# Performance work log

Hardware: AMD Instinct MI355X
Metric: run time of the kernel (lower is better)

The kernel has to match this reference:

```python
import jax, jax.numpy as jnp
import numpy as np

N = 100_000   # nodes
E = 1_600_000 # edges (avg degree 16)
IN_DIM = 128
OUT_DIM = 64
NEG_SLOPE = 0.2  # PyG GATConv default


def setup_inputs() -> dict:
    key = jax.random.key(0)
    k_x, k_ei, k_w, k_as, k_ad = jax.random.split(key, 5)
    x = jax.random.normal(k_x, (N, IN_DIM), dtype=jnp.float32)
    edge_index = jax.random.randint(k_ei, (2, E), 0, N, dtype=jnp.int32)
    # GATConv params (heads=1): linear weight, attention vectors, output bias
    W = jax.random.normal(k_w, (IN_DIM, OUT_DIM), dtype=jnp.float32) / np.sqrt(IN_DIM)
    a_src = jax.random.normal(k_as, (OUT_DIM,), dtype=jnp.float32) * 0.1
    a_dst = jax.random.normal(k_ad, (OUT_DIM,), dtype=jnp.float32) * 0.1
    bias = jnp.zeros((OUT_DIM,), dtype=jnp.float32)
    return {"x": x, "edge_index": edge_index, "W": W, "a_src": a_src, "a_dst": a_dst, "bias": bias}


def reference(x, edge_index, W, a_src, a_dst, bias):
    # PyG GATConv, heads=1, add_self_loops=True
    h = x @ W                                   # [N, OUT]
    loop = jnp.arange(N, dtype=edge_index.dtype)
    ei = jnp.concatenate([edge_index, jnp.stack([loop, loop])], axis=1)  # [2, E+N]
    src, dst = ei[0], ei[1]
    # per-node attention logits, gathered per edge
    alpha_s = h @ a_src                         # [N]
    alpha_d = h @ a_dst                         # [N]
    e = alpha_s[src] + alpha_d[dst]             # [E+N]
    e = jnp.where(e > 0, e, NEG_SLOPE * e)      # leaky_relu
    # segment softmax over edges sharing the same destination node
    m = jax.ops.segment_max(e, dst, num_segments=N)   # every node has a self loop
    ex = jnp.exp(e - m[dst])
    s = jax.ops.segment_sum(ex, dst, num_segments=N)
    alpha = ex / s[dst]                         # [E+N]
    # weighted scatter-add of source messages
    out = jax.ops.segment_sum(alpha[:, None] * h[src], dst, num_segments=N)  # [N, OUT]
    return out + bias
```

## Files before the change

### kernel.cpp

```cpp
#include <hip/hip_runtime.h>
#include <hip/hip_bf16.h>

#ifndef NEG_SLOPE
#define NEG_SLOPE 0.2f
#endif

#define GRP_SHIFT 9
#define GRP_SIZE 512
#define NGMAX 256
#define MS_CHUNK 4096
#define BKT_CAP 10240

typedef short bf16x8 __attribute__((ext_vector_type(8)));
typedef float f32x4 __attribute__((ext_vector_type(4)));

__device__ __forceinline__ unsigned short f2bf(float f) {
    union { float f; unsigned int u; } c; c.f = f;
    unsigned int r = (c.u + 0x7FFFu + ((c.u >> 16) & 1u)) >> 16;
    return (unsigned short)r;
}
__device__ __forceinline__ float bf2f(unsigned short u) {
    union { unsigned int u; float f; } c; c.u = ((unsigned int)u) << 16;
    return c.f;
}
__device__ __forceinline__ float bflo(unsigned int u) {
    union { unsigned int u; float f; } c; c.u = u << 16;
    return c.f;
}
__device__ __forceinline__ float bfhi(unsigned int u) {
    union { unsigned int u; float f; } c; c.u = u & 0xffff0000u;
    return c.f;
}

struct MsSmem {
    unsigned int pack[MS_CHUNK];
    unsigned char gtag[MS_CHUNK];
    int hist[NGMAX];
    int gb[NGMAX];
    int wsum[4];
};

__global__ __launch_bounds__(256) void ms_kernel(
    const int* __restrict__ ei, const float* __restrict__ W,
    unsigned short* __restrict__ wb, int* __restrict__ cursor,
    unsigned int* __restrict__ pairs, int E, int NG, int nchunk)
{
    __shared__ MsSmem sm;
    const int tid = threadIdx.x;

    if ((int)blockIdx.x == nchunk) {
        for (int idx = tid; idx < 8192; idx += 256) {
            const int n = idx >> 7;
            const int k = idx & 127;
            wb[idx] = f2bf(W[k * 64 + n]);
        }
        return;
    }

    unsigned int* ls_pack = sm.pack;
    unsigned char* ls_g = sm.gtag;
    int* ls_hist = sm.hist;
    int* ls_gb = sm.gb;
    int* ls_wsum = sm.wsum;

    const int cs = (int)blockIdx.x * MS_CHUNK;
    const int n = min(MS_CHUNK, E - cs);
    const int* srcp = ei + cs;
    const int* dstp = ei + E + cs;

    ls_hist[tid] = 0;
    __syncthreads();
    for (int i = tid; i < n; i += 256)
        atomicAdd(&ls_hist[dstp[i] >> GRP_SHIFT], 1);
    __syncthreads();

    const int h = ls_hist[tid];
    const int lane = tid & 63;
    int incl = h;
#pragma unroll
    for (int off = 1; off < 64; off <<= 1) {
        const int t = __shfl_up(incl, off);
        if (lane >= off) incl += t;
    }
    const int wv = tid >> 6;
    if (lane == 63) ls_wsum[wv] = incl;
    __syncthreads();
    int wpre = 0;
    for (int w = 0; w < wv; ++w) wpre += ls_wsum[w];
    const int excl = wpre + incl - h;
    if (tid < NG && h > 0) {
        const int old = atomicAdd(&cursor[tid], h);
        ls_gb[tid] = tid * BKT_CAP + old - excl;
    }
    __syncthreads();
    ls_hist[tid] = excl;
    __syncthreads();

    for (int i = tid; i < n; i += 256) {
        const int src = srcp[i];
        const int dst = dstp[i];
        const int g = dst >> GRP_SHIFT;
        const int idx = atomicAdd(&ls_hist[g], 1);
        ls_pack[idx] = ((unsigned int)src << GRP_SHIFT) | (unsigned int)(dst & (GRP_SIZE - 1));
        ls_g[idx] = (unsigned char)g;
    }
    __syncthreads();

    for (int i = tid; i < n; i += 256) {
        const int g = ls_g[i];
        const int pos = ls_gb[g] + i;
        if (pos < (g + 1) * BKT_CAP)
            pairs[pos] = ls_pack[i];
    }
}

__global__ __launch_bounds__(1024) void group_sort_kernel(
    const unsigned int* __restrict__ pairs, const int* __restrict__ cursor,
    unsigned int* __restrict__ meta, int* __restrict__ csr, int N)
{
    __shared__ int sdeg[GRP_SIZE];
    __shared__ int scur[GRP_SIZE];
    __shared__ int swsum[8];
    __shared__ int ssrc[BKT_CAP];
    const int g = blockIdx.x;
    const int tid = threadIdx.x;
    const int eb0 = g * BKT_CAP;
    const int cnt = min(cursor[g], BKT_CAP);

    if (tid < GRP_SIZE) sdeg[tid] = 0;
    __syncthreads();
    for (int i = tid; i < cnt; i += 1024)
        atomicAdd(&sdeg[pairs[eb0 + i] & (GRP_SIZE - 1)], 1);
    __syncthreads();

    int s = 0, incl = 0;
    if (tid < GRP_SIZE) {
        s = sdeg[tid];
        const int lane = tid & 63;
        incl = s;
#pragma unroll
        for (int off = 1; off < 64; off <<= 1) {
            const int t = __shfl_up(incl, off);
            if (lane >= off) incl += t;
        }
        if (lane == 63) swsum[tid >> 6] = incl;
    }
    __syncthreads();
    if (tid < GRP_SIZE) {
        int wpre = 0;
        const int wv = tid >> 6;
        for (int w = 0; w < wv; ++w) wpre += swsum[w];
        const int excl = wpre + incl - s;
        scur[tid] = excl;
        const int node = (g << GRP_SHIFT) + tid;
        if (node < N)
            meta[node] = ((unsigned int)(eb0 + excl) << 10) | (unsigned int)min(s, 1023);
    }
    __syncthreads();

    for (int i = tid; i < cnt; i += 1024) {
        const unsigned int p = pairs[eb0 + i];
        const int idx = atomicAdd(&scur[p & (GRP_SIZE - 1)], 1);
        ssrc[idx] = (int)(p >> GRP_SHIFT);
    }
    __syncthreads();
    for (int i = tid; i < cnt; i += 1024)
        csr[eb0 + i] = ssrc[i];
}

__global__ __launch_bounds__(256) void gemm_kernel(
    const float* __restrict__ x, const unsigned short* __restrict__ wb,
    const float* __restrict__ a_src, const float* __restrict__ a_dst,
    unsigned short* __restrict__ hb, float* __restrict__ as_,
    float* __restrict__ ad_, int N)
{
    __shared__ unsigned short xb[64 * 136];
    const int tid = threadIdx.x;
    const int r0 = (int)blockIdx.x * 64;

    for (int idx = tid; idx < 2048; idx += 256) {
        const int r = idx >> 5;
        const int c4 = idx & 31;
        const int row = r0 + r;
        float4 v = make_float4(0.f, 0.f, 0.f, 0.f);
        if (row < N) v = ((const float4*)(x + (size_t)row * 128))[c4];
        ushort4 o;
        o.x = f2bf(v.x); o.y = f2bf(v.y); o.z = f2bf(v.z); o.w = f2bf(v.w);
        *(ushort4*)(xb + r * 136 + c4 * 4) = o;
    }
    __syncthreads();

    const int wv = tid >> 6;
    const int lane = tid & 63;
    const int m16 = lane & 15;
    const int quad = lane >> 4;

    f32x4 acc[4];
#pragma unroll
    for (int ct = 0; ct < 4; ++ct) acc[ct] = (f32x4){0.f, 0.f, 0.f, 0.f};

    const unsigned short* xrow = xb + (wv * 16 + m16) * 136;
#pragma unroll
    for (int kq = 0; kq < 4; ++kq) {
        const int k0 = kq * 32;
        const bf16x8 a = *(const bf16x8*)(xrow + k0 + quad * 8);
#pragma unroll
        for (int ct = 0; ct < 4; ++ct) {
            const bf16x8 b = *(const bf16x8*)(wb + (ct * 16 + m16) * 128 + k0 + quad * 8);
            acc[ct] = __builtin_amdgcn_mfma_f32_16x16x32_bf16(a, b, acc[ct], 0, 0, 0);
        }
    }

#pragma unroll
    for (int ct = 0; ct < 4; ++ct) {
#pragma unroll
        for (int rg = 0; rg < 4; ++rg) {
            const int row = r0 + wv * 16 + quad * 4 + rg;
            if (row < N) hb[(size_t)row * 64 + ct * 16 + m16] = f2bf(acc[ct][rg]);
        }
    }

    float asv[4], adv[4];
#pragma unroll
    for (int ct = 0; ct < 4; ++ct) {
        asv[ct] = a_src[ct * 16 + m16];
        adv[ct] = a_dst[ct * 16 + m16];
    }
#pragma unroll
    for (int rg = 0; rg < 4; ++rg) {
        float ps = acc[0][rg] * asv[0] + acc[1][rg] * asv[1] +
                   acc[2][rg] * asv[2] + acc[3][rg] * asv[3];
        float pd = acc[0][rg] * adv[0] + acc[1][rg] * adv[1] +
                   acc[2][rg] * adv[2] + acc[3][rg] * adv[3];
#pragma unroll
        for (int off = 1; off < 16; off <<= 1) {
            ps += __shfl_xor(ps, off);
            pd += __shfl_xor(pd, off);
        }
        const int row = r0 + wv * 16 + quad * 4 + rg;
        if (m16 == 0 && row < N) { as_[row] = ps; ad_[row] = pd; }
    }
}

__device__ void aggregate_slow(
    const unsigned short* __restrict__ h, const float* __restrict__ as_,
    const float* __restrict__ ad_, const int* __restrict__ csr,
    const float* __restrict__ bias, float* __restrict__ out,
    int wid, int p0, int deg, int lane)
{
    const float adi = ad_[wid];
    float e0 = as_[wid] + adi;
    e0 = e0 > 0.f ? e0 : NEG_SLOPE * e0;
    float m = e0, ll = 1.f;
    float acc = bf2f(h[(size_t)wid * 64 + lane]);
    const int p1 = p0 + deg;
    for (int p = p0; p < p1; ++p) {
        const int sj = csr[p];
        float ee = as_[sj] + adi;
        ee = ee > 0.f ? ee : NEG_SLOPE * ee;
        const float nm = fmaxf(m, ee);
        const float sc = __expf(m - nm);
        const float pp = __expf(ee - nm);
        ll = ll * sc + pp;
        acc = acc * sc + pp * bf2f(h[(size_t)sj * 64 + lane]);
        m = nm;
    }
    out[(size_t)wid * 64 + lane] = acc / ll + bias[lane];
}

__global__ __launch_bounds__(256) void aggregate_kernel(
    const unsigned short* __restrict__ h, const float* __restrict__ as_,
    const float* __restrict__ ad_, const unsigned int* __restrict__ meta,
    const int* __restrict__ csr, const float* __restrict__ bias,
    float* __restrict__ out, int N)
{
    const int wbase = (blockIdx.x * 256 + threadIdx.x) >> 6;
    const int lane = threadIdx.x & 63;
    const int widA = wbase * 2;
    if (widA >= N) return;
    const int widB = widA + 1;
    const bool hasB = (widB < N);

    const unsigned int mtA = meta[widA];
    const unsigned int mtB = hasB ? meta[widB] : 0u;
    const int p0A = (int)(mtA >> 10), degA = (int)(mtA & 1023u);
    const int p0B = (int)(mtB >> 10), degB = (int)(mtB & 1023u);

    if (degA <= 63 && degB <= 63) {
        const float adiA = ad_[widA];
        const float adiB = hasB ? ad_[widB] : 0.f;
        float e0A = as_[widA] + adiA;
        e0A = e0A > 0.f ? e0A : NEG_SLOPE * e0A;
        float e0B = hasB ? as_[widB] + adiB : 0.f;
        e0B = e0B > 0.f ? e0B : NEG_SLOPE * e0B;

        int sA = widA, sB = hasB ? widB : widA;
        float eA = -1e30f, eB = -1e30f;
        if (lane < degA) {
            sA = csr[p0A + lane];
            const float t = as_[sA] + adiA;
            eA = t > 0.f ? t : NEG_SLOPE * t;
        } else if (lane == degA) {
            eA = e0A;
        }
        if (hasB) {
            if (lane < degB) {
                sB = csr[p0B + lane];
                const float t = as_[sB] + adiB;
                eB = t > 0.f ? t : NEG_SLOPE * t;
            } else if (lane == degB) {
                eB = e0B;
            }
        }

        float mA = eA, mB = eB;
#pragma unroll
        for (int off = 1; off < 64; off <<= 1) {
            mA = fmaxf(mA, __shfl_xor(mA, off));
            mB = fmaxf(mB, __shfl_xor(mB, off));
        }
        const float peA = __expf(eA - mA);
        const float peB = hasB ? __expf(eB - mB) : 0.f;
        float lA = peA, lB = peB;
#pragma unroll
        for (int off = 1; off < 64; off <<= 1) {
            lA += __shfl_xor(lA, off);
            lB += __shfl_xor(lB, off);
        }

        const int half = lane >> 5;
        const int l5 = lane & 31;
        const unsigned int* hb32 = (const unsigned int*)h;
        float a0 = 0.f, a1 = 0.f, b0 = 0.f, b1 = 0.f;
        const int npA = (degA + 2) >> 1;
        const int npB = hasB ? (degB + 2) >> 1 : 0;
        const int npMax = max(npA, npB);

        for (int jp = 0; jp < npMax; jp += 4) {
            const int sl0 = (jp    ) * 2 + half;
            const int sl1 = (jp + 1) * 2 + half;
            const int sl2 = (jp + 2) * 2 + half;
            const int sl3 = (jp + 3) * 2 + half;
            const int sa0 = __shfl(sA, sl0), sa1 = __shfl(sA, sl1);
            const int sa2 = __shfl(sA, sl2), sa3 = __shfl(sA, sl3);
            const int sb0 = __shfl(sB, sl0), sb1 = __shfl(sB, sl1);
            const int sb2 = __shfl(sB, sl2), sb3 = __shfl(sB, sl3);
            const float wa0 = __shfl(peA, sl0), wa1 = __shfl(peA, sl1);
            const float wa2 = __shfl(peA, sl2), wa3 = __shfl(peA, sl3);
            const float wb0 = __shfl(peB, sl0), wb1 = __shfl(peB, sl1);
            const float wb2 = __shfl(peB, sl2), wb3 = __shfl(peB, sl3);
            const unsigned int ua0 = hb32[sa0 * 32 + l5];
            const unsigned int ua1 = hb32[sa1 * 32 + l5];
            const unsigned int ua2 = hb32[sa2 * 32 + l5];
            const unsigned int ua3 = hb32[sa3 * 32 + l5];
            const unsigned int ub0 = hb32[sb0 * 32 + l5];
            const unsigned int ub1 = hb32[sb1 * 32 + l5];
            const unsigned int ub2 = hb32[sb2 * 32 + l5];
            const unsigned int ub3 = hb32[sb3 * 32 + l5];
            a0 += wa0 * bflo(ua0); a1 += wa0 * bfhi(ua0);
            a0 += wa1 * bflo(ua1); a1 += wa1 * bfhi(ua1);
            a0 += wa2 * bflo(ua2); a1 += wa2 * bfhi(ua2);
            a0 += wa3 * bflo(ua3); a1 += wa3 * bfhi(ua3);
            b0 += wb0 * bflo(ub0); b1 += wb0 * bfhi(ub0);
            b0 += wb1 * bflo(ub1); b1 += wb1 * bfhi(ub1);
            b0 += wb2 * bflo(ub2); b1 += wb2 * bfhi(ub2);
            b0 += wb3 * bflo(ub3); b1 += wb3 * bfhi(ub3);
        }
        a0 += __shfl_xor(a0, 32);
        a1 += __shfl_xor(a1, 32);
        b0 += __shfl_xor(b0, 32);
        b1 += __shfl_xor(b1, 32);
        if (half == 0) {
            const float2 bv = ((const float2*)bias)[l5];
            float2 oA;
            oA.x = a0 / lA + bv.x;
            oA.y = a1 / lA + bv.y;
            ((float2*)(out + (size_t)widA * 64))[l5] = oA;
            if (hasB) {
                float2 oB;
                oB.x = b0 / lB + bv.x;
                oB.y = b1 / lB + bv.y;
                ((float2*)(out + (size_t)widB * 64))[l5] = oB;
            }
        }
    } else {
        aggregate_slow(h, as_, ad_, csr, bias, out, widA, p0A, degA, lane);
        if (hasB) aggregate_slow(h, as_, ad_, csr, bias, out, widB, p0B, degB, lane);
    }
}

extern "C" void kernel_launch(void* const* d_in, const int* in_sizes, int n_in,
                              void* d_out, int out_size, void* d_ws, size_t ws_size,
                              hipStream_t stream)
{
    const float* x     = (const float*)d_in[0];
    const int*   ei    = (const int*)d_in[1];
    const float* W     = (const float*)d_in[2];
    const float* a_src = (const float*)d_in[3];
    const float* a_dst = (const float*)d_in[4];
    const float* bias  = (const float*)d_in[5];
    float* out = (float*)d_out;

    const int N = in_sizes[0] / 128;
    const int E = in_sizes[1] / 2;
    const int NG = (N + GRP_SIZE - 1) >> GRP_SHIFT;
    const int nchunk = (E + MS_CHUNK - 1) / MS_CHUNK;
    const int gemmBlocks = (N + 63) / 64;

    unsigned short* hb = (unsigned short*)d_ws;
    float* alpha_s = (float*)(hb + (size_t)N * 64);
    float* alpha_d = alpha_s + N;
    int* cursor = (int*)(alpha_d + N);
    unsigned int* meta = (unsigned int*)(cursor + NG);
    int* csr = (int*)(meta + N);
    unsigned int* pairs = (unsigned int*)(csr + (size_t)NG * BKT_CAP);
    unsigned short* wbuf = (unsigned short*)(pairs + (size_t)NG * BKT_CAP);

    hipMemsetAsync(cursor, 0, (size_t)NG * sizeof(int), stream);
    ms_kernel<<<nchunk + 1, 256, 0, stream>>>(ei, W, wbuf, cursor, pairs,
                                              E, NG, nchunk);
    group_sort_kernel<<<NG, 1024, 0, stream>>>(pairs, cursor, meta, csr, N);
    gemm_kernel<<<gemmBlocks, 256, 0, stream>>>(x, wbuf, a_src, a_dst, hb,
                                                alpha_s, alpha_d, N);
    aggregate_kernel<<<(N + 7) / 8, 256, 0, stream>>>(hb, alpha_s, alpha_d, meta,
                                                      csr, bias, out, N);
}
```

Baseline: 191.9 us.

## Merge group sort and GEMM into one launch with smaller dst groups

The group-sort and GEMM kernels are combined into one launch. Block index selects either bucket sorting or the x@W tile, so both phases can run concurrently and one launch is saved. Destination groups shrink from 512 to 256 nodes with smaller chunks and buckets, which gives more sort blocks with less shared memory each. The global bucket cursors are padded to separate cache lines to reduce atomic contention. The GEMM tile is split across 8 waves and combines partial attention dots through shared memory. Smaller bucket capacity raises the risk of overflow on skewed degree distributions.

```diff
diff --git a/kernel.cpp b/kernel.cpp
--- a/kernel.cpp
+++ b/kernel.cpp
@@ -5,11 +5,12 @@
 #define NEG_SLOPE 0.2f
 #endif
 
-#define GRP_SHIFT 9
-#define GRP_SIZE 512
-#define NGMAX 256
-#define MS_CHUNK 4096
-#define BKT_CAP 10240
+#define GRP_SHIFT 8
+#define GRP_SIZE 256
+#define NGMAX 512
+#define MS_CHUNK 2048
+#define BKT_CAP 5376
+#define CUR_STRIDE 16
 
 typedef short bf16x8 __attribute__((ext_vector_type(8)));
 typedef float f32x4 __attribute__((ext_vector_type(4)));
@@ -32,36 +33,26 @@
     return c.f;
 }
 
-struct MsSmem {
-    unsigned int pack[MS_CHUNK];
-    unsigned char gtag[MS_CHUNK];
-    int hist[NGMAX];
-    int gb[NGMAX];
-    int wsum[4];
-};
-
-__global__ __launch_bounds__(256) void ms_kernel(
+__global__ __launch_bounds__(512) void ms_kernel(
     const int* __restrict__ ei, const float* __restrict__ W,
     unsigned short* __restrict__ wb, int* __restrict__ cursor,
     unsigned int* __restrict__ pairs, int E, int NG, int nchunk)
 {
-    __shared__ MsSmem sm;
+    __shared__ unsigned int ls_pack[MS_CHUNK];
+    __shared__ unsigned short ls_g[MS_CHUNK];
+    __shared__ int ls_hist[NGMAX];
+    __shared__ int ls_gb[NGMAX];
+    __shared__ int ls_wsum[8];
     const int tid = threadIdx.x;
 
     if ((int)blockIdx.x == nchunk) {
-        for (int idx = tid; idx < 8192; idx += 256) {
+        for (int idx = tid; idx < 8192; idx += 512) {
             const int n = idx >> 7;
             const int k = idx & 127;
             wb[idx] = f2bf(W[k * 64 + n]);
         }
         return;
     }
-
-    unsigned int* ls_pack = sm.pack;
-    unsigned char* ls_g = sm.gtag;
-    int* ls_hist = sm.hist;
-    int* ls_gb = sm.gb;
-    int* ls_wsum = sm.wsum;
 
     const int cs = (int)blockIdx.x * MS_CHUNK;
     const int n = min(MS_CHUNK, E - cs);
@@ -70,7 +61,7 @@
 
     ls_hist[tid] = 0;
     __syncthreads();
-    for (int i = tid; i < n; i += 256)
+    for (int i = tid; i < n; i += 512)
         atomicAdd(&ls_hist[dstp[i] >> GRP_SHIFT], 1);
     __syncthreads();
 
@@ -89,24 +80,24 @@
     for (int w = 0; w < wv; ++w) wpre += ls_wsum[w];
     const int excl = wpre + incl - h;
     if (tid < NG && h > 0) {
-        const int old = atomicAdd(&cursor[tid], h);
+        const int old = atomicAdd(&cursor[tid * CUR_STRIDE], h);
         ls_gb[tid] = tid * BKT_CAP + old - excl;
     }
     __syncthreads();
     ls_hist[tid] = excl;
     __syncthreads();
 
-    for (int i = tid; i < n; i += 256) {
+    for (int i = tid; i < n; i += 512) {
         const int src = srcp[i];
         const int dst = dstp[i];
         const int g = dst >> GRP_SHIFT;
         const int idx = atomicAdd(&ls_hist[g], 1);
         ls_pack[idx] = ((unsigned int)src << GRP_SHIFT) | (unsigned int)(dst & (GRP_SIZE - 1));
-        ls_g[idx] = (unsigned char)g;
-    }
-    __syncthreads();
-
-    for (int i = tid; i < n; i += 256) {
+        ls_g[idx] = (unsigned short)g;
+    }
+    __syncthreads();
+
+    for (int i = tid; i < n; i += 512) {
         const int g = ls_g[i];
         const int pos = ls_gb[g] + i;
         if (pos < (g + 1) * BKT_CAP)
@@ -114,131 +105,167 @@
     }
 }
 
-__global__ __launch_bounds__(1024) void group_sort_kernel(
+struct SortSmem {
+    int sdeg[GRP_SIZE];
+    int scur[GRP_SIZE];
+    int swsum[4];
+    int ssrc[BKT_CAP];
+};
+struct GemmSmem {
+    unsigned short xb[64 * 136];
+    float psb[64];
+    float pdb[64];
+};
+union SgSmem { SortSmem s; GemmSmem g; };
+
+__global__ __launch_bounds__(512) void sortgemm_kernel(
     const unsigned int* __restrict__ pairs, const int* __restrict__ cursor,
-    unsigned int* __restrict__ meta, int* __restrict__ csr, int N)
-{
-    __shared__ int sdeg[GRP_SIZE];
-    __shared__ int scur[GRP_SIZE];
-    __shared__ int swsum[8];
-    __shared__ int ssrc[BKT_CAP];
-    const int g = blockIdx.x;
-    const int tid = threadIdx.x;
-    const int eb0 = g * BKT_CAP;
-    const int cnt = min(cursor[g], BKT_CAP);
-
-    if (tid < GRP_SIZE) sdeg[tid] = 0;
-    __syncthreads();
-    for (int i = tid; i < cnt; i += 1024)
-        atomicAdd(&sdeg[pairs[eb0 + i] & (GRP_SIZE - 1)], 1);
-    __syncthreads();
-
-    int s = 0, incl = 0;
-    if (tid < GRP_SIZE) {
-        s = sdeg[tid];
-        const int lane = tid & 63;
-        incl = s;
-#pragma unroll
-        for (int off = 1; off < 64; off <<= 1) {
-            const int t = __shfl_up(incl, off);
-            if (lane >= off) incl += t;
-        }
-        if (lane == 63) swsum[tid >> 6] = incl;
-    }
-    __syncthreads();
-    if (tid < GRP_SIZE) {
-        int wpre = 0;
-        const int wv = tid >> 6;
-        for (int w = 0; w < wv; ++w) wpre += swsum[w];
-        const int excl = wpre + incl - s;
-        scur[tid] = excl;
-        const int node = (g << GRP_SHIFT) + tid;
-        if (node < N)
-            meta[node] = ((unsigned int)(eb0 + excl) << 10) | (unsigned int)min(s, 1023);
-    }
-    __syncthreads();
-
-    for (int i = tid; i < cnt; i += 1024) {
-        const unsigned int p = pairs[eb0 + i];
-        const int idx = atomicAdd(&scur[p & (GRP_SIZE - 1)], 1);
-        ssrc[idx] = (int)(p >> GRP_SHIFT);
-    }
-    __syncthreads();
-    for (int i = tid; i < cnt; i += 1024)
-        csr[eb0 + i] = ssrc[i];
-}
-
-__global__ __launch_bounds__(256) void gemm_kernel(
+    unsigned int* __restrict__ meta, int* __restrict__ csr,
     const float* __restrict__ x, const unsigned short* __restrict__ wb,
     const float* __restrict__ a_src, const float* __restrict__ a_dst,
     unsigned short* __restrict__ hb, float* __restrict__ as_,
-    float* __restrict__ ad_, int N)
+    float* __restrict__ ad_, int N, int NG)
 {
-    __shared__ unsigned short xb[64 * 136];
+    __shared__ SgSmem sm;
     const int tid = threadIdx.x;
-    const int r0 = (int)blockIdx.x * 64;
-
-    for (int idx = tid; idx < 2048; idx += 256) {
-        const int r = idx >> 5;
-        const int c4 = idx & 31;
-        const int row = r0 + r;
-        float4 v = make_float4(0.f, 0.f, 0.f, 0.f);
-        if (row < N) v = ((const float4*)(x + (size_t)row * 128))[c4];
-        ushort4 o;
-        o.x = f2bf(v.x); o.y = f2bf(v.y); o.z = f2bf(v.z); o.w = f2bf(v.w);
-        *(ushort4*)(xb + r * 136 + c4 * 4) = o;
-    }
-    __syncthreads();
-
-    const int wv = tid >> 6;
-    const int lane = tid & 63;
-    const int m16 = lane & 15;
-    const int quad = lane >> 4;
-
-    f32x4 acc[4];
-#pragma unroll
-    for (int ct = 0; ct < 4; ++ct) acc[ct] = (f32x4){0.f, 0.f, 0.f, 0.f};
-
-    const unsigned short* xrow = xb + (wv * 16 + m16) * 136;
-#pragma unroll
-    for (int kq = 0; kq < 4; ++kq) {
-        const int k0 = kq * 32;
-        const bf16x8 a = *(const bf16x8*)(xrow + k0 + quad * 8);
-#pragma unroll
-        for (int ct = 0; ct < 4; ++ct) {
-            const bf16x8 b = *(const bf16x8*)(wb + (ct * 16 + m16) * 128 + k0 + quad * 8);
-            acc[ct] = __builtin_amdgcn_mfma_f32_16x16x32_bf16(a, b, acc[ct], 0, 0, 0);
-        }
-    }
-
-#pragma unroll
-    for (int ct = 0; ct < 4; ++ct) {
+
+    if ((int)blockIdx.x < NG) {
+        int* sdeg = sm.s.sdeg;
+        int* scur = sm.s.scur;
+        int* swsum = sm.s.swsum;
+        int* ssrc = sm.s.ssrc;
+        const int g = blockIdx.x;
+        const int eb0 = g * BKT_CAP;
+        const int cnt = min(cursor[g * CUR_STRIDE], BKT_CAP);
+
+        if (tid < GRP_SIZE) sdeg[tid] = 0;
+        __syncthreads();
+        for (int i = tid; i < cnt; i += 512)
+            atomicAdd(&sdeg[pairs[eb0 + i] & (GRP_SIZE - 1)], 1);
+        __syncthreads();
+
+        int s = 0, incl = 0;
+        if (tid < GRP_SIZE) {
+            s = sdeg[tid];
+            const int lane = tid & 63;
+            incl = s;
+#pragma unroll
+            for (int off = 1; off < 64; off <<= 1) {
+                const int t = __shfl_up(incl, off);
+                if (lane >= off) incl += t;
+            }
+            if (lane == 63) swsum[tid >> 6] = incl;
+        }
+        __syncthreads();
+        if (tid < GRP_SIZE) {
+            int wpre = 0;
+            const int wv = tid >> 6;
+            for (int w = 0; w < wv; ++w) wpre += swsum[w];
+            const int excl = wpre + incl - s;
+            scur[tid] = excl;
+            const int node = (g << GRP_SHIFT) + tid;
+            if (node < N)
+                meta[node] = ((unsigned int)(eb0 + excl) << 10) | (unsigned int)min(s, 1023);
+        }
+        __syncthreads();
+
+        for (int i = tid; i < cnt; i += 512) {
+            const unsigned int p = pairs[eb0 + i];
+            const int idx = atomicAdd(&scur[p & (GRP_SIZE - 1)], 1);
+            ssrc[idx] = (int)(p >> GRP_SHIFT);
+        }
+        __syncthreads();
+        for (int i = tid; i < cnt; i += 512)
+            csr[eb0 + i] = ssrc[i];
+    } else {
+        unsigned short* xb = sm.g.xb;
+        float* psb = sm.g.psb;
+        float* pdb = sm.g.pdb;
+        const int r0 = ((int)blockIdx.x - NG) * 64;
+
+        for (int idx = tid; idx < 2048; idx += 512) {
+            const int r = idx >> 5;
+            const int c4 = idx & 31;
+            const int row = r0 + r;
+            float4 v = make_float4(0.f, 0.f, 0.f, 0.f);
+            if (row < N) v = ((const float4*)(x + (size_t)row * 128))[c4];
+            ushort4 o;
+            o.x = f2bf(v.x); o.y = f2bf(v.y); o.z = f2bf(v.z); o.w = f2bf(v.w);
+            *(ushort4*)(xb + r * 136 + c4 * 4) = o;
+        }
+        __syncthreads();
+
+        const int wv = tid >> 6;
+        const int lane = tid & 63;
+        const int rq = wv >> 1;
+        const int ch = wv & 1;
+        const int m16 = lane & 15;
+        const int quad = lane >> 4;
+
+        f32x4 acc[2];
+#pragma unroll
+        for (int c = 0; c < 2; ++c) acc[c] = (f32x4){0.f, 0.f, 0.f, 0.f};
+
+        const unsigned short* xrow = xb + (rq * 16 + m16) * 136;
+#pragma unroll
+        for (int kq = 0; kq < 4; ++kq) {
+            const int k0 = kq * 32;
+            const bf16x8 a = *(const bf16x8*)(xrow + k0 + quad * 8);
+#pragma unroll
+            for (int c = 0; c < 2; ++c) {
+                const int ct = ch * 2 + c;
+                const bf16x8 b = *(const bf16x8*)(wb + (ct * 16 + m16) * 128 + k0 + quad * 8);
+                acc[c] = __builtin_amdgcn_mfma_f32_16x16x32_bf16(a, b, acc[c], 0, 0, 0);
+            }
+        }
+
+#pragma unroll
+        for (int c = 0; c < 2; ++c) {
+            const int ct = ch * 2 + c;
+#pragma unroll
+            for (int rg = 0; rg < 4; ++rg) {
+                const int row = r0 + rq * 16 + quad * 4 + rg;
+                if (row < N) hb[(size_t)row * 64 + ct * 16 + m16] = f2bf(acc[c][rg]);
+            }
+        }
+
+        float asv[2], adv[2];
+#pragma unroll
+        for (int c = 0; c < 2; ++c) {
+            asv[c] = a_src[(ch * 2 + c) * 16 + m16];
+            adv[c] = a_dst[(ch * 2 + c) * 16 + m16];
+        }
+        float psr[4], pdr[4];
 #pragma unroll
         for (int rg = 0; rg < 4; ++rg) {
-            const int row = r0 + wv * 16 + quad * 4 + rg;
-            if (row < N) hb[(size_t)row * 64 + ct * 16 + m16] = f2bf(acc[ct][rg]);
-        }
-    }
-
-    float asv[4], adv[4];
-#pragma unroll
-    for (int ct = 0; ct < 4; ++ct) {
-        asv[ct] = a_src[ct * 16 + m16];
-        adv[ct] = a_dst[ct * 16 + m16];
-    }
-#pragma unroll
-    for (int rg = 0; rg < 4; ++rg) {
-        float ps = acc[0][rg] * asv[0] + acc[1][rg] * asv[1] +
-                   acc[2][rg] * asv[2] + acc[3][rg] * asv[3];
-        float pd = acc[0][rg] * adv[0] + acc[1][rg] * adv[1] +
-                   acc[2][rg] * adv[2] + acc[3][rg] * adv[3];
-#pragma unroll
-        for (int off = 1; off < 16; off <<= 1) {
-            ps += __shfl_xor(ps, off);
-            pd += __shfl_xor(pd, off);
-        }
-        const int row = r0 + wv * 16 + quad * 4 + rg;
-        if (m16 == 0 && row < N) { as_[row] = ps; ad_[row] = pd; }
+            float ps = acc[0][rg] * asv[0] + acc[1][rg] * asv[1];
+            float pd = acc[0][rg] * adv[0] + acc[1][rg] * adv[1];
+#pragma unroll
+            for (int off = 1; off < 16; off <<= 1) {
+                ps += __shfl_xor(ps, off);
+                pd += __shfl_xor(pd, off);
+            }
+            psr[rg] = ps; pdr[rg] = pd;
+        }
+        if (ch == 0 && m16 == 0) {
+#pragma unroll
+            for (int rg = 0; rg < 4; ++rg) {
+                const int il = rq * 16 + quad * 4 + rg;
+                psb[il] = psr[rg]; pdb[il] = pdr[rg];
+            }
+        }
+        __syncthreads();
+        if (ch == 1 && m16 == 0) {
+#pragma unroll
+            for (int rg = 0; rg < 4; ++rg) {
+                const int il = rq * 16 + quad * 4 + rg;
+                const int row = r0 + il;
+                if (row < N) {
+                    as_[row] = psr[rg] + psb[il];
+                    ad_[row] = pdr[rg] + pdb[il];
+                }
+            }
+        }
     }
 }
 
@@ -411,17 +438,17 @@
     float* alpha_s = (float*)(hb + (size_t)N * 64);
     float* alpha_d = alpha_s + N;
     int* cursor = (int*)(alpha_d + N);
-    unsigned int* meta = (unsigned int*)(cursor + NG);
+    unsigned int* meta = (unsigned int*)(cursor + (size_t)NG * CUR_STRIDE);
     int* csr = (int*)(meta + N);
     unsigned int* pairs = (unsigned int*)(csr + (size_t)NG * BKT_CAP);
     unsigned short* wbuf = (unsigned short*)(pairs + (size_t)NG * BKT_CAP);
 
-    hipMemsetAsync(cursor, 0, (size_t)NG * sizeof(int), stream);
-    ms_kernel<<<nchunk + 1, 256, 0, stream>>>(ei, W, wbuf, cursor, pairs,
+    hipMemsetAsync(cursor, 0, (size_t)NG * CUR_STRIDE * sizeof(int), stream);
+    ms_kernel<<<nchunk + 1, 512, 0, stream>>>(ei, W, wbuf, cursor, pairs,
                                               E, NG, nchunk);
-    group_sort_kernel<<<NG, 1024, 0, stream>>>(pairs, cursor, meta, csr, N);
-    gemm_kernel<<<gemmBlocks, 256, 0, stream>>>(x, wbuf, a_src, a_dst, hb,
-                                                alpha_s, alpha_d, N);
+    sortgemm_kernel<<<NG + gemmBlocks, 512, 0, stream>>>(
+        pairs, cursor, meta, csr, x, wbuf, a_src, a_dst, hb,
+        alpha_s, alpha_d, N, NG);
     aggregate_kernel<<<(N + 7) / 8, 256, 0, stream>>>(hb, alpha_s, alpha_d, meta,
                                                       csr, bias, out, N);
 }
```

After: 197.0 us. 1.03x slower.
